# Optimization experiments

Hardware: AMD Instinct MI355X
Metric: run time of the kernel (lower is better)

Reference implementation:

```python
import jax, jax.numpy as jnp
import numpy as np

N_NODES = 50000
N_EDGES = 800000
D_FEAT = 64
H = 128


def scatter_mean(x, idx, num_segments):
    # mean of x rows per segment; empty segments -> 0 (matches torch_scatter scatter_mean)
    s = jax.ops.segment_sum(x, idx, num_segments=num_segments)
    c = jax.ops.segment_sum(jnp.ones((x.shape[0],), dtype=x.dtype), idx, num_segments=num_segments)
    return s / jnp.maximum(c, 1.0)[:, None]


def setup_inputs() -> dict:
    key = jax.random.key(0)
    ks = jax.random.split(key, 6)
    edge_attr = jax.random.normal(ks[0], (N_EDGES, D_FEAT), dtype=jnp.float32)
    edge_index = jax.random.randint(ks[1], (2, N_EDGES), 0, N_NODES, dtype=jnp.int64 if jax.config.jax_enable_x64 else jnp.int32)
    # ensure max index == N_NODES - 1 so num_nodes inference matches
    edge_index = edge_index.at[0, 0].set(N_NODES - 1)
    sc = 0.05
    W0 = jax.random.normal(ks[2], (D_FEAT + D_FEAT, H), dtype=jnp.float32) * sc
    b0 = jnp.zeros((H,), dtype=jnp.float32)
    W1 = jax.random.normal(ks[3], (H + D_FEAT, H), dtype=jnp.float32) * sc
    b1 = jnp.zeros((H,), dtype=jnp.float32)
    Wf = jax.random.normal(ks[4], (2 * H, 1), dtype=jnp.float32) * sc
    bf = jnp.zeros((1,), dtype=jnp.float32)
    return {"edge_attr": edge_attr, "edge_index": edge_index,
            "W0": W0, "b0": b0, "W1": W1, "b1": b1, "Wf": Wf, "bf": bf}


def reference(edge_attr, edge_index, W0, b0, W1, b1, Wf, bf):
    src = edge_index[0]
    dst = edge_index[1]
    # initial node features: mean of incoming edge_attr over edge_index[1]
    node_attr = scatter_mean(edge_attr, dst, N_NODES)            # [N, D_FEAT]
    # layer 0: aggregate over edge_index[0], concat, linear, sigmoid
    agg = scatter_mean(edge_attr, src, N_NODES)                  # [N, D_FEAT]
    node_attr = jax.nn.sigmoid(jnp.concatenate([node_attr, agg], axis=1) @ W0 + b0)  # [N, H]
    # layer 1
    agg = scatter_mean(edge_attr, src, N_NODES)                  # [N, D_FEAT]
    node_attr = jax.nn.sigmoid(jnp.concatenate([node_attr, agg], axis=1) @ W1 + b1)  # [N, H]
    # final edge classifier: gather endpoints, concat, linear
    edge_embs = jnp.concatenate([node_attr[src], node_attr[dst]], axis=1)  # [E, 2H]
    embeddings = jax.lax.stop_gradient(edge_embs)
    logits = (edge_embs @ Wf + bf).reshape(-1)                   # [E]
    return logits, embeddings
```

## Files before the change

### kernel.cpp

```cpp
#include <hip/hip_runtime.h>
#include <hip/hip_bf16.h>

#define N_NODES 50000
#define N_EDGES 800000
#define D_FEAT 64
#define H 128
#define CAP 96

typedef float f32x4 __attribute__((ext_vector_type(4)));

__global__ void k_fill(const int* __restrict__ ei,
                       int* __restrict__ cnt_dst, int* __restrict__ cnt_src,
                       int* __restrict__ bkt_dst, int* __restrict__ bkt_src) {
    int t = blockIdx.x * blockDim.x + threadIdx.x;
    if (t >= N_EDGES / 4) return;
    int4 s = ((const int4*)ei)[t];
    int4 d = ((const int4*)(ei + N_EDGES))[t];
    int e = 4 * t;
    int p;
    p = atomicAdd(&cnt_src[s.x], 1); if (p < CAP) bkt_src[(size_t)s.x * CAP + p] = e;
    p = atomicAdd(&cnt_src[s.y], 1); if (p < CAP) bkt_src[(size_t)s.y * CAP + p] = e + 1;
    p = atomicAdd(&cnt_src[s.z], 1); if (p < CAP) bkt_src[(size_t)s.z * CAP + p] = e + 2;
    p = atomicAdd(&cnt_src[s.w], 1); if (p < CAP) bkt_src[(size_t)s.w * CAP + p] = e + 3;
    p = atomicAdd(&cnt_dst[d.x], 1); if (p < CAP) bkt_dst[(size_t)d.x * CAP + p] = e;
    p = atomicAdd(&cnt_dst[d.y], 1); if (p < CAP) bkt_dst[(size_t)d.y * CAP + p] = e + 1;
    p = atomicAdd(&cnt_dst[d.z], 1); if (p < CAP) bkt_dst[(size_t)d.z * CAP + p] = e + 2;
    p = atomicAdd(&cnt_dst[d.w], 1); if (p < CAP) bkt_dst[(size_t)d.w * CAP + p] = e + 3;
}

__global__ __launch_bounds__(128) void k_node(const float* __restrict__ ea,
        const int* __restrict__ cnt_dst, const int* __restrict__ bkt_dst,
        const int* __restrict__ cnt_src, const int* __restrict__ bkt_src,
        const float* __restrict__ W0, const float* __restrict__ b0,
        const float* __restrict__ W1, const float* __restrict__ b1,
        const float* __restrict__ Wf,
        float* __restrict__ emb, float* __restrict__ ps, float* __restrict__ pd) {
    __shared__ float x0[16][128];
    __shared__ float x1[16][192];
    __shared__ float red[16][2][2];
    __shared__ int ccnt[32];
    int t = threadIdx.x;
    int n0 = blockIdx.x * 16;

    {
        int unit = t >> 2;
        int l = t & 3;
        int nn = unit >> 1;
        int dir = unit & 1;
        int n = n0 + nn;
        const int* cnt = dir ? cnt_src : cnt_dst;
        const int* bkt = dir ? bkt_src : bkt_dst;
        int c = cnt[n];
        int cc = c < CAP ? c : CAP;
        size_t b = (size_t)n * CAP;
        f32x4 a0 = {0.f,0.f,0.f,0.f}, a1 = {0.f,0.f,0.f,0.f};
        f32x4 a2 = {0.f,0.f,0.f,0.f}, a3 = {0.f,0.f,0.f,0.f};
        int i = 0;
        for (; i + 2 <= cc; i += 2) {
            int e0 = bkt[b + i];
            int e1 = bkt[b + i + 1];
            const float* r0 = ea + (size_t)e0 * D_FEAT;
            const float* r1 = ea + (size_t)e1 * D_FEAT;
            f32x4 u0 = *(const f32x4*)(r0 + 4 * l);
            f32x4 u1 = *(const f32x4*)(r0 + 4 * l + 16);
            f32x4 u2 = *(const f32x4*)(r0 + 4 * l + 32);
            f32x4 u3 = *(const f32x4*)(r0 + 4 * l + 48);
            f32x4 w0 = *(const f32x4*)(r1 + 4 * l);
            f32x4 w1 = *(const f32x4*)(r1 + 4 * l + 16);
            f32x4 w2 = *(const f32x4*)(r1 + 4 * l + 32);
            f32x4 w3 = *(const f32x4*)(r1 + 4 * l + 48);
            a0 += u0; a1 += u1; a2 += u2; a3 += u3;
            a0 += w0; a1 += w1; a2 += w2; a3 += w3;
        }
        if (i < cc) {
            int e0 = bkt[b + i];
            const float* r0 = ea + (size_t)e0 * D_FEAT;
            a0 += *(const f32x4*)(r0 + 4 * l);
            a1 += *(const f32x4*)(r0 + 4 * l + 16);
            a2 += *(const f32x4*)(r0 + 4 * l + 32);
            a3 += *(const f32x4*)(r0 + 4 * l + 48);
        }
        float dinv = 1.0f / fmaxf((float)c, 1.0f);
        a0 *= dinv; a1 *= dinv; a2 *= dinv; a3 *= dinv;
        float* xr = &x0[nn][dir * 64 + 4 * l];
        *(f32x4*)(xr)      = a0;
        *(f32x4*)(xr + 16) = a1;
        *(f32x4*)(xr + 32) = a2;
        *(f32x4*)(xr + 48) = a3;
        if (dir) {
            float* yr = &x1[nn][128 + 4 * l];
            *(f32x4*)(yr)      = a0;
            *(f32x4*)(yr + 16) = a1;
            *(f32x4*)(yr + 32) = a2;
            *(f32x4*)(yr + 48) = a3;
        }
        if (l == 0) ccnt[unit] = cc;
    }
    __syncthreads();
    {
        float acc[16];
        float bias = b0[t];
        #pragma unroll
        for (int n = 0; n < 16; n++) acc[n] = bias;
        for (int k = 0; k < 128; k += 4) {
            float w0 = W0[(k + 0) * 128 + t];
            float w1 = W0[(k + 1) * 128 + t];
            float w2 = W0[(k + 2) * 128 + t];
            float w3 = W0[(k + 3) * 128 + t];
            #pragma unroll
            for (int n = 0; n < 16; n++) {
                f32x4 xv = *(const f32x4*)&x0[n][k];
                acc[n] = fmaf(xv.x, w0, acc[n]);
                acc[n] = fmaf(xv.y, w1, acc[n]);
                acc[n] = fmaf(xv.z, w2, acc[n]);
                acc[n] = fmaf(xv.w, w3, acc[n]);
            }
        }
        #pragma unroll
        for (int n = 0; n < 16; n++) x1[n][t] = 1.0f / (1.0f + __expf(-acc[n]));
    }
    __syncthreads();
    float hv[16];
    {
        float acc[16];
        float bias = b1[t];
        #pragma unroll
        for (int n = 0; n < 16; n++) acc[n] = bias;
        for (int k = 0; k < 192; k += 4) {
            float w0 = W1[(k + 0) * 128 + t];
            float w1 = W1[(k + 1) * 128 + t];
            float w2 = W1[(k + 2) * 128 + t];
            float w3 = W1[(k + 3) * 128 + t];
            #pragma unroll
            for (int n = 0; n < 16; n++) {
                f32x4 xv = *(const f32x4*)&x1[n][k];
                acc[n] = fmaf(xv.x, w0, acc[n]);
                acc[n] = fmaf(xv.y, w1, acc[n]);
                acc[n] = fmaf(xv.z, w2, acc[n]);
                acc[n] = fmaf(xv.w, w3, acc[n]);
            }
        }
        #pragma unroll
        for (int n = 0; n < 16; n++) hv[n] = 1.0f / (1.0f + __expf(-acc[n]));
    }
    {
        float wlo = Wf[t];
        float whi = Wf[128 + t];
        int wv = t >> 6, ln = t & 63;
        #pragma unroll
        for (int n = 0; n < 16; n++) {
            float a = hv[n] * wlo;
            float b = hv[n] * whi;
            #pragma unroll
            for (int off = 32; off > 0; off >>= 1) {
                a += __shfl_xor(a, off, 64);
                b += __shfl_xor(b, off, 64);
            }
            if (ln == 0) { red[n][0][wv] = a; red[n][1][wv] = b; }
        }
    }
    __syncthreads();
    if (t < 32) {
        int n = t >> 1, half = t & 1;
        float v = red[n][half][0] + red[n][half][1];
        if (half == 0) ps[n0 + n] = v; else pd[n0 + n] = v;
    }
    int* elist = (int*)&x1[0][0];
    {
        int L = t >> 2, j0 = t & 3;
        int nn = L >> 1, dir = L & 1;
        int n = n0 + nn;
        const int* bkt = dir ? bkt_src : bkt_dst;
        int c = ccnt[L];
        for (int i = j0; i < c; i += 4)
            elist[L * CAP + i] = bkt[(size_t)n * CAP + i];
    }
    __syncthreads();
    #pragma unroll
    for (int L = 0; L < 32; L++) {
        int nn = L >> 1;
        int half = 1 - (L & 1);
        float v = hv[nn];
        int c = ccnt[L];
        const int* el = elist + L * CAP;
        size_t boff = (size_t)half * 128 + t;
        int i = 0;
        for (; i + 1 < c; i += 2) {
            int e0 = el[i], e1 = el[i + 1];
            __builtin_nontemporal_store(v, emb + (size_t)e0 * 256 + boff);
            __builtin_nontemporal_store(v, emb + (size_t)e1 * 256 + boff);
        }
        if (i < c)
            __builtin_nontemporal_store(v, emb + (size_t)el[i] * 256 + boff);
    }
}

__global__ void k_logits(const int* __restrict__ ei, const float* __restrict__ ps,
                         const float* __restrict__ pd, const float* __restrict__ bfp,
                         float* __restrict__ logits) {
    int e = blockIdx.x * blockDim.x + threadIdx.x;
    if (e >= N_EDGES) return;
    float r = ps[ei[e]] + pd[ei[N_EDGES + e]] + bfp[0];
    __builtin_nontemporal_store(r, &logits[e]);
}

extern "C" void kernel_launch(void* const* d_in, const int* in_sizes, int n_in,
                              void* d_out, int out_size, void* d_ws, size_t ws_size,
                              hipStream_t stream) {
    const float* edge_attr  = (const float*)d_in[0];
    const int*   edge_index = (const int*)d_in[1];
    const float* W0  = (const float*)d_in[2];
    const float* b0  = (const float*)d_in[3];
    const float* W1  = (const float*)d_in[4];
    const float* b1  = (const float*)d_in[5];
    const float* Wf  = (const float*)d_in[6];
    const float* bfp = (const float*)d_in[7];

    float* out = (float*)d_out;
    float* logits = out;
    float* emb    = out + N_EDGES;

    float* ws = (float*)d_ws;
    float* ps      = ws;
    float* pd      = ps + 50000;
    int*   cnt_dst = (int*)(pd + 50000);
    int*   cnt_src = cnt_dst + 50000;
    int*   bkt_dst = cnt_src + 50000;
    int*   bkt_src = bkt_dst + (size_t)N_NODES * CAP;

    hipMemsetAsync(cnt_dst, 0, 2 * N_NODES * sizeof(int), stream);

    {
        int grid = (N_EDGES / 4 + 255) / 256;
        k_fill<<<grid, 256, 0, stream>>>(edge_index, cnt_dst, cnt_src, bkt_dst, bkt_src);
    }
    {
        k_node<<<3125, 128, 0, stream>>>(edge_attr, cnt_dst, bkt_dst, cnt_src, bkt_src,
                                         W0, b0, W1, b1, Wf, emb, ps, pd);
    }
    {
        k_logits<<<3125, 256, 0, stream>>>(edge_index, ps, pd, bfp, logits);
    }
}
```

Measured before the change: 427.6 us.

## Vectorize embedding scatter with 16-byte stores and trim shared memory

```diff
diff --git a/kernel.cpp b/kernel.cpp
--- a/kernel.cpp
+++ b/kernel.cpp
@@ -8,6 +8,7 @@
 #define CAP 96
 
 typedef float f32x4 __attribute__((ext_vector_type(4)));
+typedef float f32x2 __attribute__((ext_vector_type(2)));
 
 __global__ void k_fill(const int* __restrict__ ei,
                        int* __restrict__ cnt_dst, int* __restrict__ cnt_src,
@@ -36,7 +37,7 @@
         const float* __restrict__ Wf,
         float* __restrict__ emb, float* __restrict__ ps, float* __restrict__ pd) {
     __shared__ float x0[16][128];
-    __shared__ float x1[16][192];
+    __shared__ float x1[16][128];
     __shared__ float red[16][2][2];
     __shared__ int ccnt[32];
     int t = threadIdx.x;
@@ -87,13 +88,6 @@
         *(f32x4*)(xr + 16) = a1;
         *(f32x4*)(xr + 32) = a2;
         *(f32x4*)(xr + 48) = a3;
-        if (dir) {
-            float* yr = &x1[nn][128 + 4 * l];
-            *(f32x4*)(yr)      = a0;
-            *(f32x4*)(yr + 16) = a1;
-            *(f32x4*)(yr + 32) = a2;
-            *(f32x4*)(yr + 48) = a3;
-        }
         if (l == 0) ccnt[unit] = cc;
     }
     __syncthreads();
@@ -126,7 +120,7 @@
         float bias = b1[t];
         #pragma unroll
         for (int n = 0; n < 16; n++) acc[n] = bias;
-        for (int k = 0; k < 192; k += 4) {
+        for (int k = 0; k < 128; k += 4) {
             float w0 = W1[(k + 0) * 128 + t];
             float w1 = W1[(k + 1) * 128 + t];
             float w2 = W1[(k + 2) * 128 + t];
@@ -140,6 +134,20 @@
                 acc[n] = fmaf(xv.w, w3, acc[n]);
             }
         }
+        for (int k = 128; k < 192; k += 4) {
+            float w0 = W1[(k + 0) * 128 + t];
+            float w1 = W1[(k + 1) * 128 + t];
+            float w2 = W1[(k + 2) * 128 + t];
+            float w3 = W1[(k + 3) * 128 + t];
+            #pragma unroll
+            for (int n = 0; n < 16; n++) {
+                f32x4 xv = *(const f32x4*)&x0[n][k - 64];
+                acc[n] = fmaf(xv.x, w0, acc[n]);
+                acc[n] = fmaf(xv.y, w1, acc[n]);
+                acc[n] = fmaf(xv.z, w2, acc[n]);
+                acc[n] = fmaf(xv.w, w3, acc[n]);
+            }
+        }
         #pragma unroll
         for (int n = 0; n < 16; n++) hv[n] = 1.0f / (1.0f + __expf(-acc[n]));
     }
@@ -160,48 +168,54 @@
         }
     }
     __syncthreads();
+    float (*h1s)[128] = x0;
+    #pragma unroll
+    for (int n = 0; n < 16; n++) h1s[n][t] = hv[n];
     if (t < 32) {
         int n = t >> 1, half = t & 1;
         float v = red[n][half][0] + red[n][half][1];
         if (half == 0) ps[n0 + n] = v; else pd[n0 + n] = v;
     }
-    int* elist = (int*)&x1[0][0];
-    {
-        int L = t >> 2, j0 = t & 3;
-        int nn = L >> 1, dir = L & 1;
-        int n = n0 + nn;
-        const int* bkt = dir ? bkt_src : bkt_dst;
-        int c = ccnt[L];
-        for (int i = j0; i < c; i += 4)
-            elist[L * CAP + i] = bkt[(size_t)n * CAP + i];
-    }
-    __syncthreads();
-    #pragma unroll
-    for (int L = 0; L < 32; L++) {
-        int nn = L >> 1;
-        int half = 1 - (L & 1);
-        float v = hv[nn];
-        int c = ccnt[L];
-        const int* el = elist + L * CAP;
-        size_t boff = (size_t)half * 128 + t;
-        int i = 0;
-        for (; i + 1 < c; i += 2) {
-            int e0 = el[i], e1 = el[i + 1];
-            __builtin_nontemporal_store(v, emb + (size_t)e0 * 256 + boff);
-            __builtin_nontemporal_store(v, emb + (size_t)e1 * 256 + boff);
-        }
-        if (i < c)
-            __builtin_nontemporal_store(v, emb + (size_t)el[i] * 256 + boff);
+    __syncthreads();
+    {
+        int wv = t >> 6;
+        int lane = t & 63;
+        int j = lane >> 5;
+        int q = lane & 31;
+        for (int Li = 0; Li < 16; Li++) {
+            int L = wv * 16 + Li;
+            int nn = L >> 1;
+            int dir = L & 1;
+            int half = 1 - dir;
+            const int* bl = (dir ? bkt_src : bkt_dst) + (size_t)(n0 + nn) * CAP;
+            int c = ccnt[L];
+            f32x4 hreg = *(const f32x4*)&h1s[nn][q * 4];
+            size_t boff = (size_t)half * 128 + q * 4;
+            int i = j;
+            for (; i + 2 < c; i += 4) {
+                int e0 = bl[i];
+                int e1 = bl[i + 2];
+                __builtin_nontemporal_store(hreg, (f32x4*)(emb + (size_t)e0 * 256 + boff));
+                __builtin_nontemporal_store(hreg, (f32x4*)(emb + (size_t)e1 * 256 + boff));
+            }
+            for (; i < c; i += 2) {
+                int e0 = bl[i];
+                __builtin_nontemporal_store(hreg, (f32x4*)(emb + (size_t)e0 * 256 + boff));
+            }
+        }
     }
 }
 
 __global__ void k_logits(const int* __restrict__ ei, const float* __restrict__ ps,
                          const float* __restrict__ pd, const float* __restrict__ bfp,
                          float* __restrict__ logits) {
-    int e = blockIdx.x * blockDim.x + threadIdx.x;
-    if (e >= N_EDGES) return;
-    float r = ps[ei[e]] + pd[ei[N_EDGES + e]] + bfp[0];
-    __builtin_nontemporal_store(r, &logits[e]);
+    int t = blockIdx.x * blockDim.x + threadIdx.x;
+    if (t >= N_EDGES / 2) return;
+    int2 s = ((const int2*)ei)[t];
+    int2 d = ((const int2*)(ei + N_EDGES))[t];
+    float b = bfp[0];
+    f32x2 r = { ps[s.x] + pd[d.x] + b, ps[s.y] + pd[d.y] + b };
+    __builtin_nontemporal_store(r, (f32x2*)logits + t);
 }
 
 extern "C" void kernel_launch(void* const* d_in, const int* in_sizes, int n_in,
@@ -239,6 +253,7 @@
                                          W0, b0, W1, b1, Wf, emb, ps, pd);
     }
     {
-        k_logits<<<3125, 256, 0, stream>>>(edge_index, ps, pd, bfp, logits);
-    }
-}
+        int grid = (N_EDGES / 2 + 255) / 256;
+        k_logits<<<grid, 256, 0, stream>>>(edge_index, ps, pd, bfp, logits);
+    }
+}
```

Measured after the change: 408.1 us, median of 2. 4.6% less time.
